# Optimization experiments

Measured on AMD Instinct MI355X. Metric: run time of the kernel, lower is better.

The kernel has to match this reference:

```python
import jax, jax.numpy as jnp
import numpy as np

SEQ_LEN = 2048
EMBED = 1024
HIDDEN = 1024
BATCH = 8

def setup_inputs() -> dict:
    key = jax.random.key(0)
    ks = jax.random.split(key, 7)
    scale = (6.0 / (EMBED + HIDDEN)) ** 0.5  # xavier_uniform
    inputs = jax.random.normal(ks[0], (BATCH, SEQ_LEN, EMBED), dtype=jnp.float32)
    Wq = jax.random.uniform(ks[1], (EMBED, HIDDEN), minval=-scale, maxval=scale, dtype=jnp.float32)
    Wk = jax.random.uniform(ks[2], (EMBED, HIDDEN), minval=-scale, maxval=scale, dtype=jnp.float32)
    Wv = jax.random.uniform(ks[3], (EMBED, HIDDEN), minval=-scale, maxval=scale, dtype=jnp.float32)
    bq = jax.random.normal(ks[4], (HIDDEN,), dtype=jnp.float32) * 0.01
    bk = jax.random.normal(ks[5], (HIDDEN,), dtype=jnp.float32) * 0.01
    bv = jax.random.normal(ks[6], (HIDDEN,), dtype=jnp.float32) * 0.01
    return {"inputs": inputs, "Wq": Wq, "bq": bq, "Wk": Wk, "bk": bk, "Wv": Wv, "bv": bv}

def reference(inputs, Wq, bq, Wk, bk, Wv, bv):
    # inputs: [B, S, E]
    q = jnp.einsum('bse,eh->bsh', inputs, Wq) + bq  # [B,S,H]
    k = jnp.einsum('bse,eh->bsh', inputs, Wk) + bk
    v = jnp.einsum('bse,eh->bsh', inputs, Wv) + bv
    scores = jnp.einsum('bqh,bkh->bqk', q, k) / jnp.sqrt(jnp.float32(HIDDEN))  # [B,S,S]
    causal = jnp.tril(jnp.ones((SEQ_LEN, SEQ_LEN), dtype=bool))
    scores = jnp.where(causal, scores, -jnp.inf)
    attn = jax.nn.softmax(scores, axis=-1)
    return jnp.einsum('bqk,bkh->bqh', attn, v)
```

## Files before the change

kernel.cpp:

```cpp
#include <hip/hip_runtime.h>

#define B_ 8
#define S_ 2048
#define E_ 1024
#define H_ 1024

typedef __attribute__((ext_vector_type(8))) short bf16x8;
typedef __attribute__((ext_vector_type(4))) float f32x4;

__device__ inline short f2bf(float f) {
  unsigned u = __builtin_bit_cast(unsigned, f);
  unsigned r = u + 0x7FFFu + ((u >> 16) & 1u);
  return (short)(r >> 16);
}
__device__ inline float bf2f(short s) {
  unsigned u = ((unsigned)(unsigned short)s) << 16;
  return __builtin_bit_cast(float, u);
}

__device__ inline void async16(const void* g, void* l) {
  __builtin_amdgcn_global_load_lds((const __attribute__((address_space(1))) void*)g,
                                   (__attribute__((address_space(3))) void*)l,
                                   16, 0, 0);
}

__global__ __launch_bounds__(256)
void prep(const float* __restrict__ X, short* __restrict__ Xbf,
          const float* __restrict__ W0, const float* __restrict__ W1,
          const float* __restrict__ W2, short* __restrict__ Wt) {
  __shared__ __align__(16) float t[64][65];
  const int bid = blockIdx.x;
  if (bid < 2048) {
    const int n4 = (int)((size_t)B_ * S_ * E_ / 4);
    const int stride = 2048 * 256;
    for (int i = bid * 256 + threadIdx.x; i < n4; i += stride) {
      float4 v = ((const float4*)X)[i];
      short4 o;
      o.x = f2bf(v.x); o.y = f2bf(v.y); o.z = f2bf(v.z); o.w = f2bf(v.w);
      ((short4*)Xbf)[i] = o;
    }
    return;
  }
  const int idx = bid - 2048;
  const int zz = idx >> 8;
  const int rem = idx & 255;
  const float* W = (zz == 0) ? W0 : (zz == 1) ? W1 : W2;
  short* out = Wt + (size_t)zz * H_ * E_;
  const int h0 = (rem & 15) * 64, e0 = (rem >> 4) * 64;
  const int r = threadIdx.x >> 4;
  const int c = (threadIdx.x & 15) * 4;
#pragma unroll
  for (int p = 0; p < 4; ++p) {
    int rr = r + p * 16;
    float4 v = *(const float4*)&W[(size_t)(e0 + rr) * H_ + h0 + c];
    t[rr][c + 0] = v.x; t[rr][c + 1] = v.y; t[rr][c + 2] = v.z; t[rr][c + 3] = v.w;
  }
  __syncthreads();
#pragma unroll
  for (int p = 0; p < 4; ++p) {
    int rr = r + p * 16;
    short4 o;
    o.x = f2bf(t[c + 0][rr]); o.y = f2bf(t[c + 1][rr]);
    o.z = f2bf(t[c + 2][rr]); o.w = f2bf(t[c + 3][rr]);
    *(short4*)&out[(size_t)(h0 + rr) * E_ + e0 + c] = o;
  }
}

#define BAR() asm volatile("s_barrier" ::: "memory")
#define VMC(n) asm volatile("s_waitcnt vmcnt(" #n ")" ::: "memory")

#define RD_B(buf, ks)                                                        \
  _Pragma("unroll")                                                          \
  for (int n = 0; n < 4; ++n)                                                \
    bfr[n] = *(const bf16x8*)(lBp + (buf) * 32768 + (ks) * 16384 +           \
                              ((wc * 64 + n * 16 + lr) << 6) + aCol)

#define RD_A(buf, ks, mh)                                                    \
  _Pragma("unroll")                                                          \
  for (int m = 0; m < 4; ++m)                                                \
    af[m] = *(const bf16x8*)(lAp + (buf) * 32768 + (ks) * 16384 +            \
                             ((wr * 128 + (mh) * 64 + m * 16 + lr) << 6) + aCol)

#define MFMA16(mh)                                                           \
  _Pragma("unroll")                                                          \
  for (int m = 0; m < 4; ++m) {                                              \
    _Pragma("unroll")                                                        \
    for (int n = 0; n < 4; ++n)                                              \
      acc[(mh) * 4 + m][n] = __builtin_amdgcn_mfma_f32_16x16x32_bf16(        \
          af[m], bfr[n], acc[(mh) * 4 + m][n], 0, 0, 0);                     \
  }

#define STAGE_A(buf, ks, kt) do {                                            \
    const short* _s = A + (size_t)(m0 + srow) * ldA + (kt) * 64 + (ks) * 32 + scol; \
    char* _d = (char*)lAp + (buf) * 32768 + (ks) * 16384 + wv * 1024;        \
    async16(_s, _d);                                                         \
    async16(_s + (size_t)128 * ldA, _d + 8192);                              \
  } while (0)

#define STAGE_B(buf, ks, kt) do {                                            \
    const short* _s = Bt + (size_t)(n0 + srow) * ldBt + (kt) * 64 + (ks) * 32 + scol; \
    char* _d = (char*)lBp + (buf) * 32768 + (ks) * 16384 + wv * 1024;        \
    async16(_s, _d);                                                         \
    async16(_s + (size_t)128 * ldBt, _d + 8192);                             \
  } while (0)

#define PHASE(buf, ks, mh, STG, WT) do {                                     \
    if ((mh) == 0) { RD_B(buf, ks); }                                        \
    RD_A(buf, ks, mh);                                                       \
    STG;                                                                     \
    WT;                                                                      \
    BAR();                                                                   \
    asm volatile("s_waitcnt lgkmcnt(0)" ::: "memory");                       \
    __builtin_amdgcn_sched_barrier(0);                                       \
    __builtin_amdgcn_s_setprio(1);                                           \
    MFMA16(mh);                                                              \
    __builtin_amdgcn_s_setprio(0);                                           \
    BAR();                                                                   \
  } while (0)

template <int MODE>
__global__ __launch_bounds__(512, 2)
void gemm8(const short* __restrict__ A, const short* __restrict__ Bt,
           void* __restrict__ C0, void* __restrict__ C1, void* __restrict__ C2,
           const float* __restrict__ b0, const float* __restrict__ b1,
           const float* __restrict__ b2,
           int K, int ldA, int ldBt, int ldC, float scale) {
  int bx, by;
  {
    const int bid = blockIdx.x;
    int t = (bid & 7) * 96 + (bid >> 3);
    by = t / 12; bx = t % 12;
  }

  __shared__ __align__(16) short lA[2][2][256 * 32];
  __shared__ __align__(16) short lB[2][2][256 * 32];
  const char* lAp = (const char*)&lA[0][0][0];
  const char* lBp = (const char*)&lB[0][0][0];

  const int tid = threadIdx.x;
  const int lane = tid & 63;
  const int wv = tid >> 6;
  const int wr = wv >> 2, wc = wv & 3;
  const int lr = lane & 15, kg = lane >> 4;
  const int m0 = by * 256, n0 = bx * 256;
  const int nt = K >> 6;
  const int nIter = nt >> 1;

  const int aCol = (kg * 16) ^ ((lr & 8) << 2);
  const int srow = tid >> 2;
  const int scol = (((tid & 3) * 16) ^ (tid & 32)) >> 1;

  f32x4 acc[8][4];
#pragma unroll
  for (int m = 0; m < 8; ++m)
#pragma unroll
    for (int n = 0; n < 4; ++n) acc[m][n] = (f32x4){0.f, 0.f, 0.f, 0.f};
  bf16x8 bfr[4], af[4];

  STAGE_B(0, 0, 0); STAGE_A(0, 0, 0); STAGE_B(0, 1, 0); STAGE_A(0, 1, 0);
  STAGE_B(1, 0, 1); STAGE_A(1, 0, 1); STAGE_B(1, 1, 1);
  VMC(6);
  BAR();

  for (int i = 0; i < nIter; ++i) {
    const int T = 2 * i;
    const bool lastI = (i == nIter - 1);
    PHASE(0, 0, 0, STAGE_A(1, 1, T + 1), (void)0);
    PHASE(0, 0, 1, if (!lastI) { STAGE_B(0, 0, T + 2); }, (void)0);
    PHASE(0, 1, 0, if (!lastI) { STAGE_A(0, 0, T + 2); }, (void)0);
    PHASE(0, 1, 1, if (!lastI) { STAGE_B(0, 1, T + 2); },
          if (lastI) { VMC(0); } else { VMC(6); });
    PHASE(1, 0, 0, if (!lastI) { STAGE_A(0, 1, T + 2); }, (void)0);
    PHASE(1, 0, 1, if (!lastI) { STAGE_B(1, 0, T + 3); }, (void)0);
    PHASE(1, 1, 0, if (!lastI) { STAGE_A(1, 0, T + 3); }, (void)0);
    PHASE(1, 1, 1, if (!lastI) { STAGE_B(1, 1, T + 3); },
          if (!lastI) { VMC(6); });
  }

  if ((n0 >> 10) == 2) {
    short* tv = (short*)lAp;
    const int zb = by >> 3;
    const int sb = (by & 7) * 256;
    short* VT = (short*)C2 + (size_t)zb * H_ * S_;
    const int hseg = n0 - 2048;
#pragma unroll
    for (int p = 0; p < 2; ++p) {
      if ((wc >> 1) == p) {
#pragma unroll
        for (int mq = 0; mq < 8; ++mq) {
          int sr = wr * 128 + (mq >> 2) * 64 + (mq & 3) * 16 + kg * 4;
#pragma unroll
          for (int n = 0; n < 4; ++n) {
            int c = wc * 64 + n * 16 + lr;
            float bb = b2[hseg + c];
            f32x4 v = acc[mq][n];
            short4 o;
            o.x = f2bf(v[0] + bb); o.y = f2bf(v[1] + bb);
            o.z = f2bf(v[2] + bb); o.w = f2bf(v[3] + bb);
            *(short4*)&tv[(c & 127) * 264 + sr] = o;
          }
        }
      }
      __syncthreads();
#pragma unroll
      for (int i = 0; i < 8; ++i) {
        int chunk = i * 512 + tid;
        int h = chunk >> 5, sc = (chunk & 31) * 8;
        bf16x8 v8 = *(const bf16x8*)&tv[h * 264 + sc];
        *(bf16x8*)&VT[(size_t)(hseg + p * 128 + h) * S_ + sb + sc] = v8;
      }
      __syncthreads();
    }
    return;
  }
#pragma unroll
  for (int mq = 0; mq < 8; ++mq) {
    int rowb = m0 + wr * 128 + (mq >> 2) * 64 + (mq & 3) * 16 + kg * 4;
#pragma unroll
    for (int n = 0; n < 4; ++n) {
      int col = n0 + wc * 64 + n * 16 + lr;
      f32x4 v = acc[mq][n];
      int seg = n0 >> 10;
      const float* bp = (seg == 0) ? b0 : b1;
      short* C = (short*)((seg == 0) ? C0 : C1);
      int cl = col & 1023;
      float bb = bp[cl];
#pragma unroll
      for (int r = 0; r < 4; ++r)
        C[(size_t)(rowb + r) * ldC + cl] = f2bf(v[r] + bb);
    }
  }
}


#define RD_B4(buf, ks)                                                       \
  _Pragma("unroll")                                                          \
  for (int n = 0; n < 4; ++n)                                                \
    bfr[n] = *(const bf16x8*)(lBp + (buf) * 32768 + (ks) * 16384 +           \
                              ((wc * 64 + n * 16 + lr) << 6) + aCol)

#define RD_A4(buf, ks)                                                       \
  _Pragma("unroll")                                                          \
  for (int m = 0; m < 4; ++m)                                                \
    af[m] = *(const bf16x8*)(lAp + (buf) * 16384 + (ks) * 8192 +             \
                             ((wr * 64 + m * 16 + lr) << 6) + aCol)

#define MFMA16Q()                                                            \
  _Pragma("unroll")                                                          \
  for (int m = 0; m < 4; ++m) {                                              \
    _Pragma("unroll")                                                        \
    for (int n = 0; n < 4; ++n)                                              \
      acc[m][n] = __builtin_amdgcn_mfma_f32_16x16x32_bf16(                   \
          af[m], bfr[n], acc[m][n], 0, 0, 0);                                \
  }

#define STAGE_A4(buf, ks, kt) do {                                           \
    const short* _s = A + (size_t)(m0 + srow) * ldA + (kt) * 64 + (ks) * 32 + scol; \
    char* _d = (char*)lAp + (buf) * 16384 + (ks) * 8192 + wv * 1024;         \
    async16(_s, _d);                                                         \
  } while (0)

#define STAGE_B4(buf, ks, kt) do {                                           \
    const short* _s = Bt + (size_t)(n0 + srow) * ldBt + (kt) * 64 + (ks) * 32 + scol; \
    char* _d = (char*)lBp + (buf) * 32768 + (ks) * 16384 + wv * 1024;        \
    async16(_s, _d);                                                         \
    async16(_s + (size_t)128 * ldBt, _d + 8192);                             \
  } while (0)

#define PHASE4(buf, ks, STG, WT) do {                                        \
    RD_B4(buf, ks);                                                          \
    RD_A4(buf, ks);                                                          \
    STG;                                                                     \
    WT;                                                                      \
    BAR();                                                                   \
    asm volatile("s_waitcnt lgkmcnt(0)" ::: "memory");                       \
    __builtin_amdgcn_sched_barrier(0);                                       \
    __builtin_amdgcn_s_setprio(1);                                           \
    MFMA16Q();                                                               \
    __builtin_amdgcn_s_setprio(0);                                           \
    BAR();                                                                   \
  } while (0)

template <int MODE>
__global__ __launch_bounds__(512, 2)
void gemm4(const short* __restrict__ A, const short* __restrict__ Bt,
           void* __restrict__ C0, float* __restrict__ PlO,
           int K, int ldA, int ldBt, int ldC,
           size_t zsA, size_t zsB, size_t zsC, float scale) {
  const int z = blockIdx.x & 7;
  const int rr0 = blockIdx.x >> 3;
  int bx, by;
  if (MODE == 1) {
    by = 0; int ac = 0;
    while (rr0 >= ac + (by >> 1) + 1) { ac += (by >> 1) + 1; ++by; }
    bx = rr0 - ac;
  } else {
    by = 15 - (rr0 >> 2); bx = rr0 & 3;
  }
  A  += (size_t)z * zsA;
  Bt += (size_t)z * zsB;

  __shared__ __align__(16) short lA[2][2][128 * 32];
  __shared__ __align__(16) short lB[2][2][256 * 32];
  __shared__ float sLi[128];
  const char* lAp = (const char*)&lA[0][0][0];
  const char* lBp = (const char*)&lB[0][0][0];

  const int tid = threadIdx.x;
  const int lane = tid & 63;
  const int wv = tid >> 6;
  const int wr = wv >> 2, wc = wv & 3;
  const int lr = lane & 15, kg = lane >> 4;
  const int m0 = by * 128, n0 = bx * 256;
  const int kEnd = (MODE == 2) ? ((by >> 1) + 1) * 256 : K;
  const int nt = kEnd >> 6;
  const int nIter = nt >> 1;

  const int aCol = (kg * 16) ^ ((lr & 8) << 2);
  const int srow = tid >> 2;
  const int scol = (((tid & 3) * 16) ^ (tid & 32)) >> 1;

  if (MODE == 2 && tid < 128) {
    float l = 0.f;
    for (int kt = 0; kt <= (by >> 1); ++kt)
      l += PlO[((size_t)z * 8 + kt) * S_ + m0 + tid];
    sLi[tid] = 1.f / l;
  }

  f32x4 acc[4][4];
#pragma unroll
  for (int m = 0; m < 4; ++m)
#pragma unroll
    for (int n = 0; n < 4; ++n) acc[m][n] = (f32x4){0.f, 0.f, 0.f, 0.f};
  bf16x8 bfr[4], af[4];

  STAGE_B4(0, 0, 0); STAGE_A4(0, 0, 0); STAGE_B4(0, 1, 0); STAGE_A4(0, 1, 0);
  STAGE_B4(1, 0, 1); STAGE_A4(1, 0, 1);
  VMC(6);
  if (MODE == 2) asm volatile("s_waitcnt lgkmcnt(0)" ::: "memory");
  BAR();

  for (int i = 0; i < nIter; ++i) {
    const int T = 2 * i;
    const bool lastI = (i == nIter - 1);
    PHASE4(0, 0, { STAGE_B4(1, 1, T + 1); STAGE_A4(1, 1, T + 1); }, VMC(6));
    PHASE4(0, 1, if (!lastI) { STAGE_B4(0, 0, T + 2); STAGE_A4(0, 0, T + 2); },
           if (lastI) { VMC(3); } else { VMC(6); });
    PHASE4(1, 0, if (!lastI) { STAGE_B4(0, 1, T + 2); STAGE_A4(0, 1, T + 2); },
           if (lastI) { VMC(0); } else { VMC(6); });
    PHASE4(1, 1, if (!lastI) { STAGE_B4(1, 0, T + 3); STAGE_A4(1, 0, T + 3); VMC(6); },
           (void)0);
  }

  if (MODE == 1) {
    float* tmpL = (float*)lAp;
    short* C = (short*)C0 + (size_t)z * zsC;
    const bool diag = (bx == (by >> 1));
#pragma unroll
    for (int m = 0; m < 4; ++m) {
      int rt0 = wr * 64 + m * 16 + kg * 4;
#pragma unroll
      for (int r = 0; r < 4; ++r) {
        int rt = rt0 + r;
        float se = 0.f;
#pragma unroll
        for (int n = 0; n < 4; ++n) {
          int c = wc * 64 + n * 16 + lr;
          bool ok = !diag || (n0 + c <= m0 + rt);
          short sh = ok ? f2bf(__expf(acc[m][n][r] * scale)) : (short)0;
          se += bf2f(sh);
          C[(size_t)(m0 + rt) * ldC + n0 + c] = sh;
        }
#pragma unroll
        for (int o = 1; o < 16; o <<= 1) se += __shfl_xor(se, o);
        if (lr == 0) tmpL[rt * 4 + wc] = se;
      }
    }
    __syncthreads();
    if (tid < 128) {
      float l = tmpL[tid * 4 + 0] + tmpL[tid * 4 + 1] +
                tmpL[tid * 4 + 2] + tmpL[tid * 4 + 3];
      PlO[((size_t)z * 8 + bx) * S_ + m0 + tid] = l;
    }
    return;
  }
  {
    float* C = (float*)C0 + (size_t)z * zsC;
#pragma unroll
    for (int m = 0; m < 4; ++m) {
      int rl = wr * 64 + m * 16 + kg * 4;
      f32x4 liv = *(const f32x4*)&sLi[rl];
      int rowb = m0 + rl;
#pragma unroll
      for (int n = 0; n < 4; ++n) {
        int col = n0 + wc * 64 + n * 16 + lr;
        f32x4 v = acc[m][n];
#pragma unroll
        for (int r = 0; r < 4; ++r)
          C[(size_t)(rowb + r) * ldC + col] = v[r] * liv[r];
      }
    }
  }
}

extern "C" void kernel_launch(void* const* d_in, const int* in_sizes, int n_in,
                              void* d_out, int out_size, void* d_ws, size_t ws_size,
                              hipStream_t stream) {
  const float* X  = (const float*)d_in[0];
  const float* Wq = (const float*)d_in[1];
  const float* bq = (const float*)d_in[2];
  const float* Wk = (const float*)d_in[3];
  const float* bk = (const float*)d_in[4];
  const float* Wv = (const float*)d_in[5];
  const float* bv = (const float*)d_in[6];

  char* ws = (char*)d_ws;
  const size_t MB = 1024ull * 1024ull;
  short* Pbuf = (short*)ws;
  short* Xbf  = (short*)ws;
  short* Q    = (short*)(ws + 64 * MB);
  short* Kb   = (short*)(ws + 96 * MB);
  short* Vt   = (short*)(ws + 128 * MB);
  short* Wt   = (short*)(ws + 160 * MB);
  float* Pl   = (float*)(ws + 160 * MB);

  prep<<<2816, 256, 0, stream>>>(X, Xbf, Wq, Wk, Wv, Wt);
  gemm8<0><<<768, 512, 0, stream>>>(
      Xbf, Wt, Q, Kb, Vt, bq, bk, bv, E_, E_, E_, H_, 1.f);
  gemm4<1><<<576, 512, 0, stream>>>(
      Q, Kb, Pbuf, Pl, H_, H_, H_, S_,
      (size_t)S_ * H_, (size_t)S_ * H_, (size_t)S_ * S_, 0.03125f);
  gemm4<2><<<512, 512, 0, stream>>>(
      Pbuf, Vt, d_out, Pl, S_, S_, S_, H_,
      (size_t)S_ * S_, (size_t)H_ * S_, (size_t)S_ * H_, 1.f);
}
```

Baseline: 264.0 us.

## Replace double-buffered LDS pipeline with single-buffer loop and raise occupancy hint

Removes the two-stage double-buffered async global-to-LDS prefetch pipeline from the gemm4 kernel. Each k-tile is now loaded into a single LDS buffer and waited on fully (vmcnt 0) before the MFMAs run. LDS use per block is halved, and the launch bounds hint rises from 2 to 4 blocks per CU so that occupancy, not software pipelining, is meant to hide memory latency. The cost is serialized load and compute within each block, plus tighter register limits that could cause spills with the 64-register accumulator tile.

```diff
diff --git a/kernel.cpp b/kernel.cpp
--- a/kernel.cpp
+++ b/kernel.cpp
@@ -233,16 +233,16 @@
 }
 
 
-#define RD_B4(buf, ks)                                                       \
+#define RD_B4(ks)                                                            \
   _Pragma("unroll")                                                          \
   for (int n = 0; n < 4; ++n)                                                \
-    bfr[n] = *(const bf16x8*)(lBp + (buf) * 32768 + (ks) * 16384 +           \
+    bfr[n] = *(const bf16x8*)(lBp + (ks) * 16384 +                           \
                               ((wc * 64 + n * 16 + lr) << 6) + aCol)
 
-#define RD_A4(buf, ks)                                                       \
+#define RD_A4(ks)                                                            \
   _Pragma("unroll")                                                          \
   for (int m = 0; m < 4; ++m)                                                \
-    af[m] = *(const bf16x8*)(lAp + (buf) * 16384 + (ks) * 8192 +             \
+    af[m] = *(const bf16x8*)(lAp + (ks) * 8192 +                             \
                              ((wr * 64 + m * 16 + lr) << 6) + aCol)
 
 #define MFMA16Q()                                                            \
@@ -254,35 +254,8 @@
           af[m], bfr[n], acc[m][n], 0, 0, 0);                                \
   }
 
-#define STAGE_A4(buf, ks, kt) do {                                           \
-    const short* _s = A + (size_t)(m0 + srow) * ldA + (kt) * 64 + (ks) * 32 + scol; \
-    char* _d = (char*)lAp + (buf) * 16384 + (ks) * 8192 + wv * 1024;         \
-    async16(_s, _d);                                                         \
-  } while (0)
-
-#define STAGE_B4(buf, ks, kt) do {                                           \
-    const short* _s = Bt + (size_t)(n0 + srow) * ldBt + (kt) * 64 + (ks) * 32 + scol; \
-    char* _d = (char*)lBp + (buf) * 32768 + (ks) * 16384 + wv * 1024;        \
-    async16(_s, _d);                                                         \
-    async16(_s + (size_t)128 * ldBt, _d + 8192);                             \
-  } while (0)
-
-#define PHASE4(buf, ks, STG, WT) do {                                        \
-    RD_B4(buf, ks);                                                          \
-    RD_A4(buf, ks);                                                          \
-    STG;                                                                     \
-    WT;                                                                      \
-    BAR();                                                                   \
-    asm volatile("s_waitcnt lgkmcnt(0)" ::: "memory");                       \
-    __builtin_amdgcn_sched_barrier(0);                                       \
-    __builtin_amdgcn_s_setprio(1);                                           \
-    MFMA16Q();                                                               \
-    __builtin_amdgcn_s_setprio(0);                                           \
-    BAR();                                                                   \
-  } while (0)
-
 template <int MODE>
-__global__ __launch_bounds__(512, 2)
+__global__ __launch_bounds__(512, 4)
 void gemm4(const short* __restrict__ A, const short* __restrict__ Bt,
            void* __restrict__ C0, float* __restrict__ PlO,
            int K, int ldA, int ldBt, int ldC,
@@ -300,11 +273,11 @@
   A  += (size_t)z * zsA;
   Bt += (size_t)z * zsB;
 
-  __shared__ __align__(16) short lA[2][2][128 * 32];
-  __shared__ __align__(16) short lB[2][2][256 * 32];
+  __shared__ __align__(16) short lA[2][128 * 32];
+  __shared__ __align__(16) short lB[2][256 * 32];
   __shared__ float sLi[128];
-  const char* lAp = (const char*)&lA[0][0][0];
-  const char* lBp = (const char*)&lB[0][0][0];
+  const char* lAp = (const char*)&lA[0][0];
+  const char* lBp = (const char*)&lB[0][0];
 
   const int tid = threadIdx.x;
   const int lane = tid & 63;
@@ -314,7 +287,6 @@
   const int m0 = by * 128, n0 = bx * 256;
   const int kEnd = (MODE == 2) ? ((by >> 1) + 1) * 256 : K;
   const int nt = kEnd >> 6;
-  const int nIter = nt >> 1;
 
   const int aCol = (kg * 16) ^ ((lr & 8) << 2);
   const int srow = tid >> 2;
@@ -334,22 +306,34 @@
     for (int n = 0; n < 4; ++n) acc[m][n] = (f32x4){0.f, 0.f, 0.f, 0.f};
   bf16x8 bfr[4], af[4];
 
-  STAGE_B4(0, 0, 0); STAGE_A4(0, 0, 0); STAGE_B4(0, 1, 0); STAGE_A4(0, 1, 0);
-  STAGE_B4(1, 0, 1); STAGE_A4(1, 0, 1);
-  VMC(6);
-  if (MODE == 2) asm volatile("s_waitcnt lgkmcnt(0)" ::: "memory");
-  BAR();
-
-  for (int i = 0; i < nIter; ++i) {
-    const int T = 2 * i;
-    const bool lastI = (i == nIter - 1);
-    PHASE4(0, 0, { STAGE_B4(1, 1, T + 1); STAGE_A4(1, 1, T + 1); }, VMC(6));
-    PHASE4(0, 1, if (!lastI) { STAGE_B4(0, 0, T + 2); STAGE_A4(0, 0, T + 2); },
-           if (lastI) { VMC(3); } else { VMC(6); });
-    PHASE4(1, 0, if (!lastI) { STAGE_B4(0, 1, T + 2); STAGE_A4(0, 1, T + 2); },
-           if (lastI) { VMC(0); } else { VMC(6); });
-    PHASE4(1, 1, if (!lastI) { STAGE_B4(1, 0, T + 3); STAGE_A4(1, 0, T + 3); VMC(6); },
-           (void)0);
+  for (int t = 0; t < nt; ++t) {
+    {
+      const short* sA = A + (size_t)(m0 + srow) * ldA + t * 64 + scol;
+      const short* sB = Bt + (size_t)(n0 + srow) * ldBt + t * 64 + scol;
+      char* dA = (char*)lAp + tid * 16;
+      char* dB = (char*)lBp + tid * 16;
+      async16(sA, dA);
+      async16(sA + 32, dA + 8192);
+      async16(sB, dB);
+      async16(sB + (size_t)128 * ldBt, dB + 8192);
+      async16(sB + 32, dB + 16384);
+      async16(sB + (size_t)128 * ldBt + 32, dB + 24576);
+    }
+    VMC(0);
+    BAR();
+    RD_B4(0); RD_A4(0);
+    asm volatile("s_waitcnt lgkmcnt(0)" ::: "memory");
+    __builtin_amdgcn_sched_barrier(0);
+    __builtin_amdgcn_s_setprio(1);
+    MFMA16Q();
+    __builtin_amdgcn_s_setprio(0);
+    RD_B4(1); RD_A4(1);
+    asm volatile("s_waitcnt lgkmcnt(0)" ::: "memory");
+    __builtin_amdgcn_sched_barrier(0);
+    __builtin_amdgcn_s_setprio(1);
+    MFMA16Q();
+    __builtin_amdgcn_s_setprio(0);
+    BAR();
   }
 
   if (MODE == 1) {
```

Measured after the change: 254.3 us. 3.7% less time.
